# Kernel optimization log

Hardware: AMD Instinct MI355X
Metric: run time of the kernel (lower is better)

## Reference

```python
import jax, jax.numpy as jnp
import numpy as np

B, C, T, DIN, DOUT = 8, 8, 256, 1536, 512
RADIUS = int(round(0.05 * T))  # radius = round(0.05 * Nframe)
NEG_INF = float(jnp.finfo(jnp.float32).min)


def _suppress_1d(scores):
    # Greedy temporal NMS along T for a single cine. scores: [T]
    order = jnp.argsort(-scores)  # descending
    pos = jnp.arange(T)

    def step(carry, i):
        mask, s = carry
        keep = mask[i]
        window = (jnp.abs(pos - i) <= RADIUS) & (pos != i)
        mask = jnp.where(keep, mask & ~window, mask)
        s = jnp.where(keep, s, s.at[i].set(NEG_INF))
        return (mask, s), None

    (_, s), _ = jax.lax.scan(step, (jnp.ones(T, dtype=bool), scores), order)
    return s


def _top_p_mask(scores, p):
    # scores: [B, Tflat] non-negative; returns float {0,1} mask (detached).
    s = jax.lax.stop_gradient(scores)
    s = jnp.maximum(jnp.where(jnp.isfinite(s), s, 0.0), 0.0)
    sorted_idx = jnp.argsort(-s, axis=-1)
    sorted_s = jnp.take_along_axis(s, sorted_idx, axis=-1)
    norm = sorted_s / (sorted_s.sum(axis=-1, keepdims=True) + 1e-8)
    cum = jnp.cumsum(norm, axis=-1)
    keep = cum <= p
    keep = keep.at[..., :3].set(True)  # always keep top-3
    b_idx = jnp.arange(s.shape[0])[:, None]
    mask = jnp.zeros_like(s, dtype=bool).at[b_idx, sorted_idx].set(keep)
    return mask.astype(scores.dtype)


def setup_inputs() -> dict:
    key = jax.random.key(0)
    ks = jax.random.split(key, 6)
    return {
        "query": jax.random.normal(ks[0], (B, C, T, DIN), dtype=jnp.float32),
        "values": jax.random.normal(ks[1], (B, C, T, DIN), dtype=jnp.float32),
        "W1_w": jax.random.normal(ks[2], (DIN, DOUT), dtype=jnp.float32) / np.sqrt(DIN),
        "W1_b": jax.random.normal(ks[3], (DOUT,), dtype=jnp.float32) * 0.01,
        "V_w": jax.random.normal(ks[4], (DOUT, 1), dtype=jnp.float32) / np.sqrt(DOUT),
        "V_b": jax.random.normal(ks[5], (1,), dtype=jnp.float32) * 0.01,
    }


def reference(query, values, W1_w, W1_b, V_w, V_b):
    # raw_before_suppression = V(tanh(W1(query)))  -> [B, C, T, 1]
    h = jnp.tanh(jnp.einsum('bctd,de->bcte', query, W1_w) + W1_b)
    raw_before = jnp.einsum('bcte,eo->bcto', h, V_w) + V_b

    # greedy temporal suppression, vmapped over B*C cines
    flat = raw_before[..., 0].reshape(B * C, T)
    raw = jax.vmap(_suppress_1d)(flat).reshape(B, C, T, 1)

    score = jax.nn.sigmoid(raw)
    Tflat = C * T
    flat_probs = score[..., 0].reshape(B, Tflat)
    flat_probs = jnp.where(jnp.isfinite(flat_probs), flat_probs, 0.0)

    # eval path: top_p = 0.7 nucleus mask (detached)
    mask = _top_p_mask(flat_probs, 0.7)
    mask = (mask > 0).astype(flat_probs.dtype)

    masked_score = (flat_probs * mask).reshape(B, C, T, 1)
    sum_score = jnp.sum(masked_score, axis=(1, 2), keepdims=True)
    attn = masked_score / (sum_score + 1e-8)
    attn = jnp.where(sum_score <= 0, jnp.full_like(attn, 1.0 / Tflat), attn)

    context = jnp.sum(attn * values, axis=(1, 2))  # [B, DIN]
    return context, attn, masked_score
```

## Files before the change

### kernel.cpp

```cpp
#include <hip/hip_runtime.h>
#include <math.h>
#include <stdint.h>

#define TM 16384
#define NN 512
#define KDIM 1536
#define BM 128
#define BN 128
#define BKS 32
#define NKT 48

typedef _Float16 f16x8 __attribute__((ext_vector_type(8)));
typedef __fp16 h16x2 __attribute__((ext_vector_type(2)));
typedef float f32x4 __attribute__((ext_vector_type(4)));

__device__ __forceinline__ unsigned short f16bits(_Float16 h) {
  union { _Float16 h; unsigned short u; } cv; cv.h = h; return cv.u;
}

__device__ __forceinline__ int swz_chunk(int row, int chunk) {
  return chunk ^ ((row >> 1) & 3);
}

__device__ __forceinline__ void gload_lds16(const void* g, void* l) {
  __builtin_amdgcn_global_load_lds(
      (const __attribute__((address_space(1))) unsigned int*)g,
      (__attribute__((address_space(3))) unsigned int*)l, 16, 0, 0);
}

__global__ __launch_bounds__(256) void convert_w1_kernel(
    const float* __restrict__ W1,
    unsigned short* __restrict__ W1ws)
{
  const int kt = blockIdx.x;
  const int nb = blockIdx.y;
  const int tid = threadIdx.x;
  const int k0 = kt * BKS, n0 = nb * BN;
  const size_t tbase = ((size_t)(nb * NKT + kt) * 2) * 4096;
#pragma unroll
  for (int i = 0; i < 16; ++i) {
    int idx = tid + i * 256;
    int nn = idx & 127, kk = idx >> 7;
    float f = W1[(size_t)(k0 + kk) * NN + n0 + nn];
    _Float16 h = (_Float16)f;
    _Float16 l = (_Float16)((f - (float)h) * 2048.0f);
    int off16 = nn * 32 + (swz_chunk(nn, kk >> 3) << 3) + (kk & 7);
    W1ws[tbase + off16] = f16bits(h);
    W1ws[tbase + 4096 + off16] = f16bits(l);
  }
}

__global__ __launch_bounds__(512, 4) void gemm_score_kernel(
    const float* __restrict__ query,
    const unsigned short* __restrict__ W1ws,
    const float* __restrict__ W1b,
    const float* __restrict__ Vw,
    float* __restrict__ raw_part)
{
  __shared__ __align__(16) char ldsb[2][32768];

  const int tid = threadIdx.x;
  const int lane = tid & 63;
  const int w = tid >> 6;
  const int lrow = lane & 15;
  const int lseg = lane >> 4;

  const int bid = blockIdx.x;
  const int lin = (bid & 7) * 64 + (bid >> 3);
  const int mb = lin >> 2, nb = lin & 3;
  const int m0 = mb * BM, n0 = nb * BN;

  f32x4 zero = {0.f, 0.f, 0.f, 0.f};
  f32x4 acc[8], acc2[8];
#pragma unroll
  for (int n = 0; n < 8; ++n) { acc[n] = zero; acc2[n] = zero; }

  char* const ldsbase = &ldsb[0][0];

  const char* aG0;
  const char* aG1;
  {
    int chunk0 = (w * 2 + 0) * 64 + lane;
    int row0 = chunk0 >> 3, cp0 = chunk0 & 7;
    int kc0 = cp0 ^ (row0 & 7);
    aG0 = (const char*)(query + (size_t)(m0 + row0) * KDIM + kc0 * 4);
    int chunk1 = (w * 2 + 1) * 64 + lane;
    int row1 = chunk1 >> 3, cp1 = chunk1 & 7;
    int kc1 = cp1 ^ (row1 & 7);
    aG1 = (const char*)(query + (size_t)(m0 + row1) * KDIM + kc1 * 4);
  }
  const char* bGH = (const char*)W1ws + (size_t)(nb * NKT) * 16384
                    + w * 1024 + lane * 16;
  const char* bGL = bGH + 8192;

  const int ldsA0 = (w * 2 + 0) * 1024;
  const int ldsA1 = (w * 2 + 1) * 1024;
  const int ldsBH = 16384 + w * 1024;
  const int ldsBL = 24576 + w * 1024;
  const int rowA = w * 16 + lrow;
  const int offA0 = rowA * 128 + (((lseg * 2) ^ (rowA & 7)) << 4);
  const int offA1 = rowA * 128 + (((lseg * 2 + 1) ^ (rowA & 7)) << 4);
  int boffH[8], boffL[8];
#pragma unroll
  for (int nf = 0; nf < 8; ++nf) {
    int brow = nf * 16 + lrow;
    boffH[nf] = 16384 + brow * 64 + (swz_chunk(brow, lseg) << 4);
    boffL[nf] = boffH[nf] + 8192;
  }

  auto STAGE = [&](int bufi) {
    char* base = ldsbase + (bufi << 15);
    gload_lds16(aG0, base + ldsA0);
    gload_lds16(aG1, base + ldsA1);
    gload_lds16(bGH, base + ldsBH);
    gload_lds16(bGL, base + ldsBL);
    aG0 += BKS * 4;
    aG1 += BKS * 4;
    bGH += 16384;
    bGL += 16384;
  };

  STAGE(0);
  for (int kt = 0; kt < NKT; ++kt) {
    const int cur = kt & 1;
    if (kt + 1 < NKT) {
      STAGE(cur ^ 1);
      asm volatile("s_waitcnt vmcnt(4)" ::: "memory");
    } else {
      asm volatile("s_waitcnt vmcnt(0)" ::: "memory");
    }
    __builtin_amdgcn_s_barrier();

    const char* base = ldsbase + (cur << 15);
    f16x8 afh, afl;
    {
      f32x4 va = *reinterpret_cast<const f32x4*>(base + offA0);
      f32x4 vb = *reinterpret_cast<const f32x4*>(base + offA1);
      union H8 { f16x8 v; h16x2 p[4]; } h, l;
      h.p[0] = __builtin_amdgcn_cvt_pkrtz(va[0], va[1]);
      h.p[1] = __builtin_amdgcn_cvt_pkrtz(va[2], va[3]);
      h.p[2] = __builtin_amdgcn_cvt_pkrtz(vb[0], vb[1]);
      h.p[3] = __builtin_amdgcn_cvt_pkrtz(vb[2], vb[3]);
      float r0 = (va[0] - (float)h.p[0][0]) * 2048.0f;
      float r1 = (va[1] - (float)h.p[0][1]) * 2048.0f;
      float r2 = (va[2] - (float)h.p[1][0]) * 2048.0f;
      float r3 = (va[3] - (float)h.p[1][1]) * 2048.0f;
      float r4 = (vb[0] - (float)h.p[2][0]) * 2048.0f;
      float r5 = (vb[1] - (float)h.p[2][1]) * 2048.0f;
      float r6 = (vb[2] - (float)h.p[3][0]) * 2048.0f;
      float r7 = (vb[3] - (float)h.p[3][1]) * 2048.0f;
      l.p[0] = __builtin_amdgcn_cvt_pkrtz(r0, r1);
      l.p[1] = __builtin_amdgcn_cvt_pkrtz(r2, r3);
      l.p[2] = __builtin_amdgcn_cvt_pkrtz(r4, r5);
      l.p[3] = __builtin_amdgcn_cvt_pkrtz(r6, r7);
      afh = h.v;
      afl = l.v;
    }
    __builtin_amdgcn_s_setprio(1);
#pragma unroll
    for (int nf = 0; nf < 8; ++nf) {
      f16x8 bh = *reinterpret_cast<const f16x8*>(base + boffH[nf]);
      f16x8 bl = *reinterpret_cast<const f16x8*>(base + boffL[nf]);
      acc[nf]  = __builtin_amdgcn_mfma_f32_16x16x32_f16(afh, bh, acc[nf], 0, 0, 0);
      acc2[nf] = __builtin_amdgcn_mfma_f32_16x16x32_f16(afh, bl, acc2[nf], 0, 0, 0);
      acc2[nf] = __builtin_amdgcn_mfma_f32_16x16x32_f16(afl, bh, acc2[nf], 0, 0, 0);
    }
    __builtin_amdgcn_s_setprio(0);
    asm volatile("s_waitcnt lgkmcnt(0)" ::: "memory");
    __builtin_amdgcn_s_barrier();
  }

  float part[4] = {0.f, 0.f, 0.f, 0.f};
#pragma unroll
  for (int nf = 0; nf < 8; ++nf) {
    int col = n0 + nf * 16 + lrow;
    float bias = W1b[col];
    float vw = Vw[col];
#pragma unroll
    for (int r = 0; r < 4; ++r) {
      float z = acc[nf][r] + acc2[nf][r] * 4.8828125e-4f + bias;
      part[r] += tanhf(z) * vw;
    }
  }
#pragma unroll
  for (int off = 1; off < 16; off <<= 1)
#pragma unroll
    for (int r = 0; r < 4; ++r)
      part[r] += __shfl_xor(part[r], off, 64);
  if (lrow == 0) {
    int rowb = m0 + w * 16 + lseg * 4;
#pragma unroll
    for (int r = 0; r < 4; ++r)
      raw_part[(size_t)nb * TM + rowb + r] = part[r];
  }
}

__global__ __launch_bounds__(64) void nms_kernel(
    const float* __restrict__ raw_part,
    const float* __restrict__ Vb,
    float* __restrict__ probs)
{
  const int cine = blockIdx.x;
  const int lane = threadIdx.x;
  __shared__ float s[256];
  __shared__ int order[256];
  float sv[4];
  const float vb = Vb[0];
#pragma unroll
  for (int q = 0; q < 4; ++q) {
    int p = q * 64 + lane;
    int idx = cine * 256 + p;
    float r = vb;
#pragma unroll
    for (int sl = 0; sl < 4; ++sl) r += raw_part[sl * TM + idx];
    sv[q] = r;
    s[p] = r;
  }
  __syncthreads();
#pragma unroll
  for (int q = 0; q < 4; ++q) {
    int p = q * 64 + lane;
    float st = sv[q];
    int rk = 0;
    for (int j = 0; j < 256; ++j) {
      float sj = s[j];
      rk += (sj > st) || (sj == st && j < p);
    }
    order[rk] = p;
  }
  __syncthreads();
  unsigned m = 0xFu;
  for (int r = 0; r < 256; ++r) {
    int i = order[r];
    int qi = i >> 6, li = i & 63;
    unsigned long long ball = __ballot((lane == li) && ((m >> qi) & 1u));
    if (ball) {
#pragma unroll
      for (int q = 0; q < 4; ++q) {
        int d = q * 64 + lane - i;
        if (d != 0 && d <= 13 && d >= -13) m &= ~(1u << q);
      }
    } else if (lane == li) {
      s[i] = -3.402823466385289e+38f;
    }
  }
  __syncthreads();
#pragma unroll
  for (int q = 0; q < 4; ++q) {
    int p = q * 64 + lane;
    probs[cine * 256 + p] = 1.0f / (1.0f + expf(-s[p]));
  }
}

__global__ __launch_bounds__(256) void topp_kernel(
    const float* __restrict__ probs,
    float* __restrict__ out)
{
  const int b = blockIdx.x;
  const int tid = threadIdx.x;
  __shared__ float p[2048];
  __shared__ int cnz[2048];
  __shared__ float sv[2048];
  __shared__ int sidx[2048];
  __shared__ unsigned char msk[2048];
  __shared__ float red[256];
  __shared__ int nnz_s;

  if (tid == 0) nnz_s = 0;
  for (int i = tid; i < 2048; i += 256) {
    p[i] = probs[b * 2048 + i];
    msk[i] = 0;
  }
  __syncthreads();
  float lsum = 0.f;
  for (int i = tid; i < 2048; i += 256) {
    float v = p[i];
    lsum += v;
    if (v > 0.f) {
      int slot = atomicAdd(&nnz_s, 1);
      cnz[slot] = i;
    }
  }
  red[tid] = lsum;
  __syncthreads();
  for (int sred = 128; sred > 0; sred >>= 1) {
    if (tid < sred) red[tid] += red[tid + sred];
    __syncthreads();
  }
  const int nnz = nnz_s;
  const float total = red[0];
  for (int c = tid; c < nnz; c += 256) {
    int i = cnz[c];
    float pi = p[i];
    int rank = 0;
    for (int cc = 0; cc < nnz; ++cc) {
      int j = cnz[cc];
      float pj = p[j];
      rank += (pj > pi) || (pj == pi && j < i);
    }
    sv[rank] = pi;
    sidx[rank] = i;
  }
  __syncthreads();
  if (tid == 0) {
    float denom = total + 1e-8f;
    float cum = 0.f;
    for (int r = 0; r < nnz; ++r) {
      cum += sv[r] / denom;
      if ((cum <= 0.7f) || (r < 3)) msk[sidx[r]] = 1;
    }
  }
  __syncthreads();
  float ls = 0.f;
  for (int i = tid; i < 2048; i += 256) {
    float m = msk[i] ? p[i] : 0.f;
    sv[i] = m;
    ls += m;
  }
  red[tid] = ls;
  __syncthreads();
  for (int sred = 128; sred > 0; sred >>= 1) {
    if (tid < sred) red[tid] += red[tid + sred];
    __syncthreads();
  }
  const float ssum = red[0];
  const float denom = ssum + 1e-8f;
  const bool uni = (ssum <= 0.f);
  for (int i = tid; i < 2048; i += 256) {
    float m = sv[i];
    out[28672 + b * 2048 + i] = m;
    out[12288 + b * 2048 + i] = uni ? (1.0f / 2048.0f) : (m / denom);
  }
}

__global__ __launch_bounds__(256) void ctx_part_kernel(
    const float* __restrict__ attn,
    const float* __restrict__ values,
    float* __restrict__ ctxp)
{
  const int ch = blockIdx.x % 6;
  const int g  = (blockIdx.x / 6) & 7;
  const int b  = blockIdx.x / 48;
  const int tid = threadIdx.x;
  const int lane = tid & 63, w = tid >> 6;
  __shared__ float av[256];
  __shared__ int   idx[256];
  __shared__ int   wcnt[4];

  float a = attn[b * 2048 + g * 256 + tid];
  unsigned long long mask = __ballot(a != 0.f);
  if (lane == 0) wcnt[w] = __popcll(mask);
  __syncthreads();
  int base = 0;
  for (int i = 0; i < w; ++i) base += wcnt[i];
  if (a != 0.f) {
    int pos = base + __popcll(mask & ((1ull << lane) - 1ull));
    av[pos] = a;
    idx[pos] = g * 256 + tid;
  }
  __syncthreads();
  const int total = wcnt[0] + wcnt[1] + wcnt[2] + wcnt[3];
  const int d = ch * 256 + tid;
  float acc = 0.f;
#pragma unroll 4
  for (int t = 0; t < total; ++t)
    acc += av[t] * values[((size_t)b * 2048 + idx[t]) * KDIM + d];
  ctxp[((size_t)(b * 8 + g)) * KDIM + d] = acc;
}

__global__ __launch_bounds__(256) void ctx_reduce_kernel(
    const float* __restrict__ ctxp,
    float* __restrict__ out)
{
  const int i = blockIdx.x * 256 + threadIdx.x;
  const int b = i / KDIM, d = i % KDIM;
  float sum = 0.f;
#pragma unroll
  for (int g = 0; g < 8; ++g) sum += ctxp[((size_t)(b * 8 + g)) * KDIM + d];
  out[i] = sum;
}

extern "C" void kernel_launch(void* const* d_in, const int* in_sizes, int n_in,
                              void* d_out, int out_size, void* d_ws, size_t ws_size,
                              hipStream_t stream) {
  const float* query  = (const float*)d_in[0];
  const float* values = (const float*)d_in[1];
  const float* W1w    = (const float*)d_in[2];
  const float* W1b    = (const float*)d_in[3];
  const float* Vw     = (const float*)d_in[4];
  const float* Vb     = (const float*)d_in[5];
  float* out = (float*)d_out;

  unsigned short* W1ws = (unsigned short*)d_ws;
  float* raw_part = (float*)((char*)d_ws + 3145728);
  float* probs    = raw_part + 4 * TM;
  float* ctxp     = probs + TM;

  convert_w1_kernel<<<dim3(NKT, 4), 256, 0, stream>>>(W1w, W1ws);
  gemm_score_kernel<<<512, 512, 0, stream>>>(query, W1ws, W1b, Vw, raw_part);
  nms_kernel<<<64, 64, 0, stream>>>(raw_part, Vb, probs);
  topp_kernel<<<8, 256, 0, stream>>>(probs, out);
  ctx_part_kernel<<<384, 256, 0, stream>>>(out + 12288, values, ctxp);
  ctx_reduce_kernel<<<48, 256, 0, stream>>>(ctxp, out);
}
```

Before: 165.0 us.

## Retile GEMM waves into a 4x2 grid of 32x64 subtiles to cut LDS B reads

Changes the per-wave work split in the score GEMM. Each of 8 waves previously covered 16 rows by all 128 columns; now the waves form a 4x2 grid, each covering 32 rows by 64 columns. Each B fragment is reused across two A fragments, which halves LDS B traffic per MFMA while doubling A loads and conversions. A small shared-memory reduction combines the two column-halves' partial V-projections before the global store, adding one extra barrier.

```diff
diff --git a/kernel.cpp b/kernel.cpp
--- a/kernel.cpp
+++ b/kernel.cpp
@@ -26,6 +26,29 @@
   __builtin_amdgcn_global_load_lds(
       (const __attribute__((address_space(1))) unsigned int*)g,
       (__attribute__((address_space(3))) unsigned int*)l, 16, 0, 0);
+}
+
+__device__ __forceinline__ void conv8(const f32x4 va, const f32x4 vb,
+                                      f16x8& hh, f16x8& ll) {
+  union H8 { f16x8 v; h16x2 p[4]; } h, l;
+  h.p[0] = __builtin_amdgcn_cvt_pkrtz(va[0], va[1]);
+  h.p[1] = __builtin_amdgcn_cvt_pkrtz(va[2], va[3]);
+  h.p[2] = __builtin_amdgcn_cvt_pkrtz(vb[0], vb[1]);
+  h.p[3] = __builtin_amdgcn_cvt_pkrtz(vb[2], vb[3]);
+  float r0 = (va[0] - (float)h.p[0][0]) * 2048.0f;
+  float r1 = (va[1] - (float)h.p[0][1]) * 2048.0f;
+  float r2 = (va[2] - (float)h.p[1][0]) * 2048.0f;
+  float r3 = (va[3] - (float)h.p[1][1]) * 2048.0f;
+  float r4 = (vb[0] - (float)h.p[2][0]) * 2048.0f;
+  float r5 = (vb[1] - (float)h.p[2][1]) * 2048.0f;
+  float r6 = (vb[2] - (float)h.p[3][0]) * 2048.0f;
+  float r7 = (vb[3] - (float)h.p[3][1]) * 2048.0f;
+  l.p[0] = __builtin_amdgcn_cvt_pkrtz(r0, r1);
+  l.p[1] = __builtin_amdgcn_cvt_pkrtz(r2, r3);
+  l.p[2] = __builtin_amdgcn_cvt_pkrtz(r4, r5);
+  l.p[3] = __builtin_amdgcn_cvt_pkrtz(r6, r7);
+  hh = h.v;
+  ll = l.v;
 }
 
 __global__ __launch_bounds__(256) void convert_w1_kernel(
@@ -58,10 +81,13 @@
     float* __restrict__ raw_part)
 {
   __shared__ __align__(16) char ldsb[2][32768];
+  __shared__ float red[2][BM];
 
   const int tid = threadIdx.x;
   const int lane = tid & 63;
   const int w = tid >> 6;
+  const int wr = w & 3;
+  const int wc = w >> 2;
   const int lrow = lane & 15;
   const int lseg = lane >> 4;
 
@@ -71,9 +97,11 @@
   const int m0 = mb * BM, n0 = nb * BN;
 
   f32x4 zero = {0.f, 0.f, 0.f, 0.f};
-  f32x4 acc[8], acc2[8];
-#pragma unroll
-  for (int n = 0; n < 8; ++n) { acc[n] = zero; acc2[n] = zero; }
+  f32x4 acc[2][4], acc2[2][4];
+#pragma unroll
+  for (int m = 0; m < 2; ++m)
+#pragma unroll
+    for (int n = 0; n < 4; ++n) { acc[m][n] = zero; acc2[m][n] = zero; }
 
   char* const ldsbase = &ldsb[0][0];
 
@@ -97,16 +125,16 @@
   const int ldsA1 = (w * 2 + 1) * 1024;
   const int ldsBH = 16384 + w * 1024;
   const int ldsBL = 24576 + w * 1024;
-  const int rowA = w * 16 + lrow;
-  const int offA0 = rowA * 128 + (((lseg * 2) ^ (rowA & 7)) << 4);
-  const int offA1 = rowA * 128 + (((lseg * 2 + 1) ^ (rowA & 7)) << 4);
-  int boffH[8], boffL[8];
-#pragma unroll
-  for (int nf = 0; nf < 8; ++nf) {
-    int brow = nf * 16 + lrow;
-    boffH[nf] = 16384 + brow * 64 + (swz_chunk(brow, lseg) << 4);
-    boffL[nf] = boffH[nf] + 8192;
-  }
+  int offA[2][2];
+#pragma unroll
+  for (int m = 0; m < 2; ++m) {
+    int row = wr * 32 + m * 16 + lrow;
+#pragma unroll
+    for (int c = 0; c < 2; ++c)
+      offA[m][c] = row * 128 + (((lseg * 2 + c) ^ (lrow & 7)) << 4);
+  }
+  const int bro = 16384 + (wc * 64 + lrow) * 64
+                  + ((lseg ^ ((lrow >> 1) & 3)) << 4);
 
   auto STAGE = [&](int bufi) {
     char* base = ldsbase + (bufi << 15);
@@ -132,67 +160,66 @@
     __builtin_amdgcn_s_barrier();
 
     const char* base = ldsbase + (cur << 15);
-    f16x8 afh, afl;
-    {
-      f32x4 va = *reinterpret_cast<const f32x4*>(base + offA0);
-      f32x4 vb = *reinterpret_cast<const f32x4*>(base + offA1);
-      union H8 { f16x8 v; h16x2 p[4]; } h, l;
-      h.p[0] = __builtin_amdgcn_cvt_pkrtz(va[0], va[1]);
-      h.p[1] = __builtin_amdgcn_cvt_pkrtz(va[2], va[3]);
-      h.p[2] = __builtin_amdgcn_cvt_pkrtz(vb[0], vb[1]);
-      h.p[3] = __builtin_amdgcn_cvt_pkrtz(vb[2], vb[3]);
-      float r0 = (va[0] - (float)h.p[0][0]) * 2048.0f;
-      float r1 = (va[1] - (float)h.p[0][1]) * 2048.0f;
-      float r2 = (va[2] - (float)h.p[1][0]) * 2048.0f;
-      float r3 = (va[3] - (float)h.p[1][1]) * 2048.0f;
-      float r4 = (vb[0] - (float)h.p[2][0]) * 2048.0f;
-      float r5 = (vb[1] - (float)h.p[2][1]) * 2048.0f;
-      float r6 = (vb[2] - (float)h.p[3][0]) * 2048.0f;
-      float r7 = (vb[3] - (float)h.p[3][1]) * 2048.0f;
-      l.p[0] = __builtin_amdgcn_cvt_pkrtz(r0, r1);
-      l.p[1] = __builtin_amdgcn_cvt_pkrtz(r2, r3);
-      l.p[2] = __builtin_amdgcn_cvt_pkrtz(r4, r5);
-      l.p[3] = __builtin_amdgcn_cvt_pkrtz(r6, r7);
-      afh = h.v;
-      afl = l.v;
+    f16x8 afh[2], afl[2];
+#pragma unroll
+    for (int m = 0; m < 2; ++m) {
+      f32x4 va = *reinterpret_cast<const f32x4*>(base + offA[m][0]);
+      f32x4 vb = *reinterpret_cast<const f32x4*>(base + offA[m][1]);
+      conv8(va, vb, afh[m], afl[m]);
     }
     __builtin_amdgcn_s_setprio(1);
 #pragma unroll
-    for (int nf = 0; nf < 8; ++nf) {
-      f16x8 bh = *reinterpret_cast<const f16x8*>(base + boffH[nf]);
-      f16x8 bl = *reinterpret_cast<const f16x8*>(base + boffL[nf]);
-      acc[nf]  = __builtin_amdgcn_mfma_f32_16x16x32_f16(afh, bh, acc[nf], 0, 0, 0);
-      acc2[nf] = __builtin_amdgcn_mfma_f32_16x16x32_f16(afh, bl, acc2[nf], 0, 0, 0);
-      acc2[nf] = __builtin_amdgcn_mfma_f32_16x16x32_f16(afl, bh, acc2[nf], 0, 0, 0);
+    for (int nf = 0; nf < 4; ++nf) {
+      const char* p = base + bro + nf * 1024;
+      f16x8 bh = *reinterpret_cast<const f16x8*>(p);
+      f16x8 bl = *reinterpret_cast<const f16x8*>(p + 8192);
+#pragma unroll
+      for (int m = 0; m < 2; ++m) {
+        acc[m][nf]  = __builtin_amdgcn_mfma_f32_16x16x32_f16(afh[m], bh, acc[m][nf], 0, 0, 0);
+        acc2[m][nf] = __builtin_amdgcn_mfma_f32_16x16x32_f16(afh[m], bl, acc2[m][nf], 0, 0, 0);
+        acc2[m][nf] = __builtin_amdgcn_mfma_f32_16x16x32_f16(afl[m], bh, acc2[m][nf], 0, 0, 0);
+      }
     }
     __builtin_amdgcn_s_setprio(0);
     asm volatile("s_waitcnt lgkmcnt(0)" ::: "memory");
     __builtin_amdgcn_s_barrier();
   }
 
-  float part[4] = {0.f, 0.f, 0.f, 0.f};
-#pragma unroll
-  for (int nf = 0; nf < 8; ++nf) {
-    int col = n0 + nf * 16 + lrow;
+  float part[2][4];
+#pragma unroll
+  for (int m = 0; m < 2; ++m)
+#pragma unroll
+    for (int r = 0; r < 4; ++r) part[m][r] = 0.f;
+#pragma unroll
+  for (int nf = 0; nf < 4; ++nf) {
+    int col = n0 + wc * 64 + nf * 16 + lrow;
     float bias = W1b[col];
     float vw = Vw[col];
 #pragma unroll
-    for (int r = 0; r < 4; ++r) {
-      float z = acc[nf][r] + acc2[nf][r] * 4.8828125e-4f + bias;
-      part[r] += tanhf(z) * vw;
-    }
+    for (int m = 0; m < 2; ++m)
+#pragma unroll
+      for (int r = 0; r < 4; ++r) {
+        float z = acc[m][nf][r] + acc2[m][nf][r] * 4.8828125e-4f + bias;
+        part[m][r] += tanhf(z) * vw;
+      }
   }
 #pragma unroll
   for (int off = 1; off < 16; off <<= 1)
 #pragma unroll
-    for (int r = 0; r < 4; ++r)
-      part[r] += __shfl_xor(part[r], off, 64);
+    for (int m = 0; m < 2; ++m)
+#pragma unroll
+      for (int r = 0; r < 4; ++r)
+        part[m][r] += __shfl_xor(part[m][r], off, 64);
   if (lrow == 0) {
-    int rowb = m0 + w * 16 + lseg * 4;
-#pragma unroll
-    for (int r = 0; r < 4; ++r)
-      raw_part[(size_t)nb * TM + rowb + r] = part[r];
-  }
+#pragma unroll
+    for (int m = 0; m < 2; ++m)
+#pragma unroll
+      for (int r = 0; r < 4; ++r)
+        red[wc][wr * 32 + m * 16 + lseg * 4 + r] = part[m][r];
+  }
+  __syncthreads();
+  if (tid < BM)
+    raw_part[(size_t)nb * TM + m0 + tid] = red[0][tid] + red[1][tid];
 }
 
 __global__ __launch_bounds__(64) void nms_kernel(
```

Result: no change. 166.8 us (+1.1%).
